# Kernel optimization log

Hardware: AMD Instinct MI355X
Metric: run time of the kernel (lower is better)

## Reference

```python
import jax, jax.numpy as jnp
import numpy as np

N = 1_000_000      # occupied voxels
GRID = 256         # voxel grid extent per axis
K = 27             # 3^3 kernel offsets
CIN, COUT = 2, 16


def _build_nbr_map(coords: np.ndarray) -> np.ndarray:
    """Kernel-offset neighbor map like MinkowskiEngine's kernel map.
    coords: [N,3] unique int voxel coords. Returns [N,K] int32, -1 = no neighbor.
    """
    key = (coords[:, 0] * GRID + coords[:, 1]) * GRID + coords[:, 2]
    order = np.argsort(key)
    skey = key[order]
    offsets = np.array([[dx, dy, dz]
                        for dx in (-1, 0, 1)
                        for dy in (-1, 0, 1)
                        for dz in (-1, 0, 1)], dtype=np.int64)
    nbr = np.full((coords.shape[0], K), -1, dtype=np.int32)
    for k in range(K):
        nc = coords + offsets[k]
        valid = np.all((nc >= 0) & (nc < GRID), axis=1)
        nkey = (nc[:, 0] * GRID + nc[:, 1]) * GRID + nc[:, 2]
        pos = np.clip(np.searchsorted(skey, nkey), 0, coords.shape[0] - 1)
        hit = valid & (skey[pos] == nkey)
        nbr[:, k] = np.where(hit, order[pos].astype(np.int32), -1)
    return nbr


def setup_inputs() -> dict:
    rng = np.random.default_rng(0)
    lin = rng.choice(GRID ** 3, size=N, replace=False)  # unique voxel ids
    coords = np.stack([lin // (GRID * GRID), (lin // GRID) % GRID, lin % GRID],
                      axis=1).astype(np.int64)
    nbr = _build_nbr_map(coords)
    key = jax.random.key(0)
    k1, k2 = jax.random.split(key)
    features = jax.random.normal(k1, (N, CIN), dtype=jnp.float32)
    # MinkowskiConvolution kernel: one [Cin,Cout] matrix per kernel offset, no bias
    kernel = jax.random.normal(k2, (K, CIN, COUT), dtype=jnp.float32) * 0.1
    return {"features": features, "kernel": kernel, "nbr_idx": jnp.asarray(nbr)}


def reference(features, kernel, nbr_idx):
    # gather-GEMM-scatter sparse conv: out[n] = sum_k W_k^T x[nbr(n,k)]
    mask = (nbr_idx >= 0)
    safe = jnp.maximum(nbr_idx, 0)
    gathered = features[safe]                              # [N,K,Cin]
    gathered = gathered * mask[..., None].astype(features.dtype)
    return jnp.einsum('nkc,kcd->nd', gathered, kernel)     # [N,Cout]
```

## Files before the change

kernel.cpp:

```cpp
#include <hip/hip_runtime.h>

#define K_OFF 27
#define CIN   2
#define COUT  16
#define BLK   256
#define WPB   4
#define IPW   (64 * K_OFF)
#define NB    8

typedef __attribute__((address_space(3))) unsigned int lds_u32;
typedef __attribute__((address_space(1))) const unsigned int g_u32;

__global__ __launch_bounds__(256) void pack_feats_kernel(
    const float2* __restrict__ feats2, unsigned* __restrict__ pkf, int n)
{
    const int i = blockIdx.x * 256 + threadIdx.x;
    if (i < n) {
        const float2 f = feats2[i];
        unsigned bx = __float_as_uint(f.x);
        unsigned by = __float_as_uint(f.y);
        bx = (bx + 0x7FFFu + ((bx >> 16) & 1u)) >> 16;
        by = (by + 0x7FFFu + ((by >> 16) & 1u)) >> 16;
        pkf[i] = bx | (by << 16);
    }
}

__global__ __launch_bounds__(BLK, 2) void spconv_kernel(
    const unsigned* __restrict__ pkf,
    const float* __restrict__ w,
    const int*   __restrict__ nbr,
    float*       __restrict__ out,
    int n_pts)
{
    __shared__ int    s_idx[WPB * IPW];
    __shared__ float4 s_w[8 * K_OFF];

    const int t    = threadIdx.x;
    const int lane = t & 63;
    const int wv   = t >> 6;
    const int tile = blockIdx.x * WPB + wv;
    const int p    = tile * 64 + lane;

    if (t < 8 * K_OFF) {
        const int k = t >> 3, q = t & 7;
        s_w[q * K_OFF + k] = reinterpret_cast<const float4*>(w)[t];
    }

    const bool full = ((tile + 1) * 64 <= n_pts);
    if (full) {
        const int* src = nbr + (size_t)tile * IPW;
        int*       dst = s_idx + wv * IPW;
        #pragma unroll
        for (int j = 0; j < 6; ++j) {
            __builtin_amdgcn_global_load_lds(
                (g_u32*)(src + j * 256 + lane * 4),
                (lds_u32*)(dst + j * 256), 16, 0, 0);
        }
        if (lane < 48) {
            __builtin_amdgcn_global_load_lds(
                (g_u32*)(src + 6 * 256 + lane * 4),
                (lds_u32*)(dst + 6 * 256), 16, 0, 0);
        }
    }
    __syncthreads();

    float acc[COUT];
    #pragma unroll
    for (int d = 0; d < COUT; ++d) acc[d] = 0.f;

    const int* rowp = s_idx + wv * IPW + lane * K_OFF;

    unsigned bm = 0;
    if (full) {
        #pragma unroll
        for (int k = 0; k < K_OFF; ++k)
            bm |= (rowp[k] >= 0) ? (1u << k) : 0u;
    }

    int mx = __popc(bm);
    #pragma unroll
    for (int off = 32; off; off >>= 1) mx = max(mx, __shfl_xor(mx, off, 64));

    for (int j0 = 0; j0 < mx; j0 += NB) {
        int   kk[NB]; float fm[NB];
        #pragma unroll
        for (int j = 0; j < NB; ++j) {
            const bool alive = (bm != 0);
            kk[j] = alive ? (int)__builtin_ctz(bm) : 0;
            fm[j] = alive ? 1.0f : 0.0f;
            bm &= bm - 1;
        }
        int idx[NB];
        #pragma unroll
        for (int j = 0; j < NB; ++j) idx[j] = rowp[kk[j]];
        unsigned u[NB];
        #pragma unroll
        for (int j = 0; j < NB; ++j)
            u[j] = pkf[(fm[j] > 0.f && idx[j] > 0) ? idx[j] : 0];
        #pragma unroll
        for (int j = 0; j < NB; ++j) {
            const float fx = __uint_as_float(u[j] << 16) * fm[j];
            const float fy = __uint_as_float(u[j] & 0xFFFF0000u) * fm[j];
            const int k = kk[j];
            #pragma unroll
            for (int q = 0; q < 4; ++q) {
                const float4 wa = s_w[q * K_OFF + k];
                const float4 wb = s_w[(q + 4) * K_OFF + k];
                acc[q*4+0] = fmaf(fy, wb.x, fmaf(fx, wa.x, acc[q*4+0]));
                acc[q*4+1] = fmaf(fy, wb.y, fmaf(fx, wa.y, acc[q*4+1]));
                acc[q*4+2] = fmaf(fy, wb.z, fmaf(fx, wa.z, acc[q*4+2]));
                acc[q*4+3] = fmaf(fy, wb.w, fmaf(fx, wa.w, acc[q*4+3]));
            }
        }
    }

    if (!full) {
        const bool pv = (p < n_pts);
        for (int k = 0; k < K_OFF; ++k) {
            const int idx = pv ? nbr[(size_t)p * K_OFF + k] : -1;
            const float fm2 = (idx >= 0) ? 1.0f : 0.0f;
            const unsigned uu = pkf[idx > 0 ? idx : 0];
            const float fx = __uint_as_float(uu << 16) * fm2;
            const float fy = __uint_as_float(uu & 0xFFFF0000u) * fm2;
            #pragma unroll
            for (int q = 0; q < 4; ++q) {
                const float4 wa = s_w[q * K_OFF + k];
                const float4 wb = s_w[(q + 4) * K_OFF + k];
                acc[q*4+0] = fmaf(fy, wb.x, fmaf(fx, wa.x, acc[q*4+0]));
                acc[q*4+1] = fmaf(fy, wb.y, fmaf(fx, wa.y, acc[q*4+1]));
                acc[q*4+2] = fmaf(fy, wb.z, fmaf(fx, wa.z, acc[q*4+2]));
                acc[q*4+3] = fmaf(fy, wb.w, fmaf(fx, wa.w, acc[q*4+3]));
            }
        }
    }

    if (p < n_pts) {
        float4* o = reinterpret_cast<float4*>(out + (size_t)p * COUT);
        o[0] = make_float4(acc[0],  acc[1],  acc[2],  acc[3]);
        o[1] = make_float4(acc[4],  acc[5],  acc[6],  acc[7]);
        o[2] = make_float4(acc[8],  acc[9],  acc[10], acc[11]);
        o[3] = make_float4(acc[12], acc[13], acc[14], acc[15]);
    }
}

extern "C" void kernel_launch(void* const* d_in, const int* in_sizes, int n_in,
                              void* d_out, int out_size, void* d_ws, size_t ws_size,
                              hipStream_t stream) {
    const float* feats = (const float*)d_in[0];
    const float* w     = (const float*)d_in[1];
    const int*   nbr   = (const int*)d_in[2];
    float*       out   = (float*)d_out;
    unsigned*    pkf   = (unsigned*)d_ws;

    const int n_pts   = in_sizes[0] / CIN;
    const int n_tiles = (n_pts + 63) / 64;
    const int grid    = (n_tiles + WPB - 1) / WPB;

    pack_feats_kernel<<<(n_pts + 255) / 256, 256, 0, stream>>>(
        reinterpret_cast<const float2*>(feats), pkf, n_pts);
    spconv_kernel<<<grid, BLK, 0, stream>>>(pkf, w, nbr, out, n_pts);
}
```

Measured before the change: 53.95 us.

## Pipeline neighbor-map staging and feature gathers in a persistent warp loop

Replaces the one-tile-per-wave kernel with a persistent kernel capped at 512 blocks. Each wave loops over tiles and double-buffers the neighbor-index tile in LDS, issuing async global-to-LDS gathers of the packed features for the next tile while it computes the current one. Partial tiles move to a separate small tail kernel, which adds a launch. The aim is to hide the latency of the index loads and random feature gathers. In exchange it relies on fragile hand-written vmcnt/lgkmcnt waits, uses more LDS per block and may give less occupancy-driven parallelism.

```diff
diff --git a/kernel.cpp b/kernel.cpp
--- a/kernel.cpp
+++ b/kernel.cpp
@@ -25,122 +25,246 @@
     }
 }
 
-__global__ __launch_bounds__(BLK, 2) void spconv_kernel(
+__device__ __forceinline__ void stage_tile(const int* __restrict__ nbr,
+                                           int tile, int* dst, int lane) {
+    const int* src = nbr + (size_t)tile * IPW;
+    #pragma unroll
+    for (int j = 0; j < 6; ++j)
+        __builtin_amdgcn_global_load_lds((g_u32*)(src + j * 256 + lane * 4),
+                                         (lds_u32*)(dst + j * 256), 16, 0, 0);
+    if (lane < 48)
+        __builtin_amdgcn_global_load_lds((g_u32*)(src + 6 * 256 + lane * 4),
+                                         (lds_u32*)(dst + 6 * 256), 16, 0, 0);
+}
+
+#define SCAN_CAP_ISSUE(BUF, GB, KK, IX, NV, MX)                               \
+    {                                                                         \
+        const int* rowp_ = (BUF) + lane * K_OFF;                              \
+        unsigned b_ = 0;                                                      \
+        _Pragma("unroll")                                                     \
+        for (int k2 = 0; k2 < K_OFF; ++k2)                                    \
+            b_ |= (rowp_[k2] >= 0) ? (1u << k2) : 0u;                         \
+        NV = __popc(b_);                                                      \
+        int m_ = NV;                                                          \
+        _Pragma("unroll")                                                     \
+        for (int o_ = 32; o_; o_ >>= 1) m_ = max(m_, __shfl_xor(m_, o_, 64)); \
+        MX = m_;                                                              \
+        _Pragma("unroll")                                                     \
+        for (int j = 0; j < 2 * NB; ++j) {                                    \
+            KK[j] = (b_ != 0) ? (int)__builtin_ctz(b_) : 0;                   \
+            b_ &= b_ - 1;                                                     \
+        }                                                                     \
+        _Pragma("unroll")                                                     \
+        for (int j = 0; j < NB; ++j) {                \
+            const int ii_ = rowp_[KK[NB + j]];                                \
+            IX[j] = (NB + j < NV && ii_ > 0) ? ii_ : 0;                       \
+        }                                                                     \
+        _Pragma("unroll")                                                     \
+        for (int j = 0; j < NB; ++j) {     \
+            const int iv_ = rowp_[KK[j]];                                     \
+            const int sf_ = (j < NV && iv_ > 0) ? iv_ : 0;                    \
+            __builtin_amdgcn_global_load_lds((g_u32*)(pkf + sf_),             \
+                                             (lds_u32*)((GB) + j * 64), 4, 0, 0); \
+        }                                                                     \
+    }
+
+#define FMA_LDS(GB, KK, NV, JOFF)                                             \
+    _Pragma("unroll")                                                         \
+    for (int j = 0; j < NB; ++j) {                                            \
+        const unsigned u_ = (unsigned)(GB)[j * 64 + lane];                    \
+        const float fm_ = ((JOFF) + j < (NV)) ? 1.0f : 0.0f;                  \
+        const float fx = __uint_as_float(u_ << 16) * fm_;                     \
+        const float fy = __uint_as_float(u_ & 0xFFFF0000u) * fm_;             \
+        const int k2 = KK[(JOFF) + j];                                        \
+        _Pragma("unroll")                                                     \
+        for (int q = 0; q < 4; ++q) {                                         \
+            const float4 wa = s_w[q * K_OFF + k2];                            \
+            const float4 wb = s_w[(q + 4) * K_OFF + k2];                      \
+            acc[4*q+0] = fmaf(fy, wb.x, fmaf(fx, wa.x, acc[4*q+0]));          \
+            acc[4*q+1] = fmaf(fy, wb.y, fmaf(fx, wa.y, acc[4*q+1]));          \
+            acc[4*q+2] = fmaf(fy, wb.z, fmaf(fx, wa.z, acc[4*q+2]));          \
+            acc[4*q+3] = fmaf(fy, wb.w, fmaf(fx, wa.w, acc[4*q+3]));          \
+        }                                                                     \
+    }
+
+__global__ __launch_bounds__(BLK, 2) void spconv_pipe_kernel(
     const unsigned* __restrict__ pkf,
-    const float* __restrict__ w,
-    const int*   __restrict__ nbr,
-    float*       __restrict__ out,
-    int n_pts)
+    const float*    __restrict__ w,
+    const int*      __restrict__ nbr,
+    float*          __restrict__ out,
+    int n_tiles)
 {
-    __shared__ int    s_idx[WPB * IPW];
-    __shared__ float4 s_w[8 * K_OFF];
+    __shared__ int    s_idx[WPB * 2 * IPW];
+    __shared__ int    s_g  [WPB * 2 * NB * 64];
+    __shared__ float4 s_w  [8 * K_OFF];
 
     const int t    = threadIdx.x;
     const int lane = t & 63;
     const int wv   = t >> 6;
-    const int tile = blockIdx.x * WPB + wv;
-    const int p    = tile * 64 + lane;
 
     if (t < 8 * K_OFF) {
         const int k = t >> 3, q = t & 7;
         s_w[q * K_OFF + k] = reinterpret_cast<const float4*>(w)[t];
     }
-
-    const bool full = ((tile + 1) * 64 <= n_pts);
-    if (full) {
-        const int* src = nbr + (size_t)tile * IPW;
-        int*       dst = s_idx + wv * IPW;
+    __syncthreads();
+
+    const int wstride = gridDim.x * WPB;
+    int tile = blockIdx.x * WPB + wv;
+    if (tile >= n_tiles) return;
+
+    int* const bufA = s_idx + wv * (2 * IPW);
+    int* const bufB = bufA + IPW;
+    int* const gbA  = s_g + wv * (2 * NB * 64);
+    int* const gbB  = gbA + NB * 64;
+
+    int kk1[2 * NB], ix1[NB], nv1, mx1;
+    int kk2[2 * NB], ix2[NB], nv2, mx2;
+
+    stage_tile(nbr, tile, bufA, lane);
+    asm volatile("s_waitcnt vmcnt(0)" ::: "memory");
+    __builtin_amdgcn_sched_barrier(0);
+    SCAN_CAP_ISSUE(bufA, gbA, kk1, ix1, nv1, mx1)
+    if (tile + wstride < n_tiles) stage_tile(nbr, tile + wstride, bufB, lane);
+
+    int  cur   = 0;
+    bool first = true;
+
+    while (true) {
+        const int  nxt  = tile + wstride;
+        const bool has1 = (nxt < n_tiles);
+        const int  n2   = tile + 2 * wstride;
+        const bool has2 = (n2 < n_tiles);
+
+        int* const bufC = cur ? bufB : bufA;
+        int* const bufN = cur ? bufA : bufB;
+        int* const gbC  = cur ? gbB  : gbA;
+        int* const gbN  = cur ? gbA  : gbB;
+
+        if (first) asm volatile("s_waitcnt vmcnt(0)" ::: "memory");
+        else       asm volatile("s_waitcnt vmcnt(4)" ::: "memory");
+        first = false;
+        __builtin_amdgcn_sched_barrier(0);
+
+        const bool early_stage = has2 && (mx1 <= 2 * NB);
+        if (early_stage) stage_tile(nbr, n2, bufC, lane);
+
+        if (has1) SCAN_CAP_ISSUE(bufN, gbN, kk2, ix2, nv2, mx2)
+
+        float acc[COUT];
         #pragma unroll
-        for (int j = 0; j < 6; ++j) {
-            __builtin_amdgcn_global_load_lds(
-                (g_u32*)(src + j * 256 + lane * 4),
-                (lds_u32*)(dst + j * 256), 16, 0, 0);
+        for (int d = 0; d < COUT; ++d) acc[d] = 0.f;
+
+        FMA_LDS(gbC, kk1, nv1, 0)
+
+        if (mx1 > NB) {
+            asm volatile("s_waitcnt lgkmcnt(0)" ::: "memory");
+            __builtin_amdgcn_sched_barrier(0);
+            #pragma unroll
+            for (int j = 0; j < NB; ++j)
+                __builtin_amdgcn_global_load_lds((g_u32*)(pkf + ix1[j]),
+                                                 (lds_u32*)(gbC + j * 64), 4, 0, 0);
+            asm volatile("s_waitcnt vmcnt(0)" ::: "memory");
+            __builtin_amdgcn_sched_barrier(0);
+            FMA_LDS(gbC, kk1, nv1, NB)
+
+            if (mx1 > 2 * NB) {
+                const int* rowp_ = bufC + lane * K_OFF;
+                unsigned b_ = 0;
+                #pragma unroll
+                for (int k2 = 0; k2 < K_OFF; ++k2)
+                    b_ |= (rowp_[k2] >= 0) ? (1u << k2) : 0u;
+                #pragma unroll
+                for (int j = 0; j < 2 * NB; ++j) b_ &= b_ - 1;
+                int rem = mx1 - 2 * NB;
+                while (rem > 0) {
+                    int kkx[NB]; float fmx[NB];
+                    #pragma unroll
+                    for (int j = 0; j < NB; ++j) {
+                        const bool a_ = (b_ != 0);
+                        kkx[j] = a_ ? (int)__builtin_ctz(b_) : 0;
+                        fmx[j] = a_ ? 1.0f : 0.0f;
+                        b_ &= b_ - 1;
+                    }
+                    asm volatile("s_waitcnt lgkmcnt(0)" ::: "memory");
+                    __builtin_amdgcn_sched_barrier(0);
+                    #pragma unroll
+                    for (int j = 0; j < NB; ++j) {
+                        const int iv_ = rowp_[kkx[j]];
+                        const int sf_ = (fmx[j] > 0.f && iv_ > 0) ? iv_ : 0;
+                        __builtin_amdgcn_global_load_lds((g_u32*)(pkf + sf_),
+                                                         (lds_u32*)(gbC + j * 64), 4, 0, 0);
+                    }
+                    asm volatile("s_waitcnt vmcnt(0)" ::: "memory");
+                    __builtin_amdgcn_sched_barrier(0);
+                    #pragma unroll
+                    for (int j = 0; j < NB; ++j) {
+                        const unsigned u_ = (unsigned)gbC[j * 64 + lane];
+                        const float fx = __uint_as_float(u_ << 16) * fmx[j];
+                        const float fy = __uint_as_float(u_ & 0xFFFF0000u) * fmx[j];
+                        const int k2 = kkx[j];
+                        #pragma unroll
+                        for (int q = 0; q < 4; ++q) {
+                            const float4 wa = s_w[q * K_OFF + k2];
+                            const float4 wb = s_w[(q + 4) * K_OFF + k2];
+                            acc[4*q+0] = fmaf(fy, wb.x, fmaf(fx, wa.x, acc[4*q+0]));
+                            acc[4*q+1] = fmaf(fy, wb.y, fmaf(fx, wa.y, acc[4*q+1]));
+                            acc[4*q+2] = fmaf(fy, wb.z, fmaf(fx, wa.z, acc[4*q+2]));
+                            acc[4*q+3] = fmaf(fy, wb.w, fmaf(fx, wa.w, acc[4*q+3]));
+                        }
+                    }
+                    rem -= NB;
+                }
+                if (has2) stage_tile(nbr, n2, bufC, lane);
+            }
         }
-        if (lane < 48) {
-            __builtin_amdgcn_global_load_lds(
-                (g_u32*)(src + 6 * 256 + lane * 4),
-                (lds_u32*)(dst + 6 * 256), 16, 0, 0);
+
+        {
+            const int p = tile * 64 + lane;
+            float4* o = reinterpret_cast<float4*>(out + (size_t)p * COUT);
+            o[0] = make_float4(acc[0],  acc[1],  acc[2],  acc[3]);
+            o[1] = make_float4(acc[4],  acc[5],  acc[6],  acc[7]);
+            o[2] = make_float4(acc[8],  acc[9],  acc[10], acc[11]);
+            o[3] = make_float4(acc[12], acc[13], acc[14], acc[15]);
         }
-    }
-    __syncthreads();
-
+
+        if (!has1) break;
+
+        #pragma unroll
+        for (int j = 0; j < 2 * NB; ++j) kk1[j] = kk2[j];
+        #pragma unroll
+        for (int j = 0; j < NB; ++j) ix1[j] = ix2[j];
+        nv1 = nv2; mx1 = mx2;
+
+        tile = nxt;
+        cur ^= 1;
+    }
+}
+
+__global__ __launch_bounds__(64) void spconv_tail_kernel(
+    const unsigned* __restrict__ pkf, const float* __restrict__ w,
+    const int* __restrict__ nbr, float* __restrict__ out, int n_pts, int p0)
+{
+    const int p = p0 + threadIdx.x;
+    if (p >= n_pts) return;
     float acc[COUT];
     #pragma unroll
     for (int d = 0; d < COUT; ++d) acc[d] = 0.f;
-
-    const int* rowp = s_idx + wv * IPW + lane * K_OFF;
-
-    unsigned bm = 0;
-    if (full) {
-        #pragma unroll
-        for (int k = 0; k < K_OFF; ++k)
-            bm |= (rowp[k] >= 0) ? (1u << k) : 0u;
-    }
-
-    int mx = __popc(bm);
-    #pragma unroll
-    for (int off = 32; off; off >>= 1) mx = max(mx, __shfl_xor(mx, off, 64));
-
-    for (int j0 = 0; j0 < mx; j0 += NB) {
-        int   kk[NB]; float fm[NB];
-        #pragma unroll
-        for (int j = 0; j < NB; ++j) {
-            const bool alive = (bm != 0);
-            kk[j] = alive ? (int)__builtin_ctz(bm) : 0;
-            fm[j] = alive ? 1.0f : 0.0f;
-            bm &= bm - 1;
+    for (int k = 0; k < K_OFF; ++k) {
+        const int idx = nbr[(size_t)p * K_OFF + k];
+        if (idx >= 0) {
+            const unsigned u = pkf[idx];
+            const float fx = __uint_as_float(u << 16);
+            const float fy = __uint_as_float(u & 0xFFFF0000u);
+            #pragma unroll
+            for (int d = 0; d < COUT; ++d)
+                acc[d] = fmaf(fy, w[k * 32 + 16 + d], fmaf(fx, w[k * 32 + d], acc[d]));
         }
-        int idx[NB];
-        #pragma unroll
-        for (int j = 0; j < NB; ++j) idx[j] = rowp[kk[j]];
-        unsigned u[NB];
-        #pragma unroll
-        for (int j = 0; j < NB; ++j)
-            u[j] = pkf[(fm[j] > 0.f && idx[j] > 0) ? idx[j] : 0];
-        #pragma unroll
-        for (int j = 0; j < NB; ++j) {
-            const float fx = __uint_as_float(u[j] << 16) * fm[j];
-            const float fy = __uint_as_float(u[j] & 0xFFFF0000u) * fm[j];
-            const int k = kk[j];
-            #pragma unroll
-            for (int q = 0; q < 4; ++q) {
-                const float4 wa = s_w[q * K_OFF + k];
-                const float4 wb = s_w[(q + 4) * K_OFF + k];
-                acc[q*4+0] = fmaf(fy, wb.x, fmaf(fx, wa.x, acc[q*4+0]));
-                acc[q*4+1] = fmaf(fy, wb.y, fmaf(fx, wa.y, acc[q*4+1]));
-                acc[q*4+2] = fmaf(fy, wb.z, fmaf(fx, wa.z, acc[q*4+2]));
-                acc[q*4+3] = fmaf(fy, wb.w, fmaf(fx, wa.w, acc[q*4+3]));
-            }
-        }
-    }
-
-    if (!full) {
-        const bool pv = (p < n_pts);
-        for (int k = 0; k < K_OFF; ++k) {
-            const int idx = pv ? nbr[(size_t)p * K_OFF + k] : -1;
-            const float fm2 = (idx >= 0) ? 1.0f : 0.0f;
-            const unsigned uu = pkf[idx > 0 ? idx : 0];
-            const float fx = __uint_as_float(uu << 16) * fm2;
-            const float fy = __uint_as_float(uu & 0xFFFF0000u) * fm2;
-            #pragma unroll
-            for (int q = 0; q < 4; ++q) {
-                const float4 wa = s_w[q * K_OFF + k];
-                const float4 wb = s_w[(q + 4) * K_OFF + k];
-                acc[q*4+0] = fmaf(fy, wb.x, fmaf(fx, wa.x, acc[q*4+0]));
-                acc[q*4+1] = fmaf(fy, wb.y, fmaf(fx, wa.y, acc[q*4+1]));
-                acc[q*4+2] = fmaf(fy, wb.z, fmaf(fx, wa.z, acc[q*4+2]));
-                acc[q*4+3] = fmaf(fy, wb.w, fmaf(fx, wa.w, acc[q*4+3]));
-            }
-        }
-    }
-
-    if (p < n_pts) {
-        float4* o = reinterpret_cast<float4*>(out + (size_t)p * COUT);
-        o[0] = make_float4(acc[0],  acc[1],  acc[2],  acc[3]);
-        o[1] = make_float4(acc[4],  acc[5],  acc[6],  acc[7]);
-        o[2] = make_float4(acc[8],  acc[9],  acc[10], acc[11]);
-        o[3] = make_float4(acc[12], acc[13], acc[14], acc[15]);
-    }
+    }
+    float4* o = reinterpret_cast<float4*>(out + (size_t)p * COUT);
+    o[0] = make_float4(acc[0],  acc[1],  acc[2],  acc[3]);
+    o[1] = make_float4(acc[4],  acc[5],  acc[6],  acc[7]);
+    o[2] = make_float4(acc[8],  acc[9],  acc[10], acc[11]);
+    o[3] = make_float4(acc[12], acc[13], acc[14], acc[15]);
 }
 
 extern "C" void kernel_launch(void* const* d_in, const int* in_sizes, int n_in,
@@ -152,11 +276,18 @@
     float*       out   = (float*)d_out;
     unsigned*    pkf   = (unsigned*)d_ws;
 
-    const int n_pts   = in_sizes[0] / CIN;
-    const int n_tiles = (n_pts + 63) / 64;
-    const int grid    = (n_tiles + WPB - 1) / WPB;
+    const int n_pts  = in_sizes[0] / CIN;
+    const int n_full = n_pts / 64;
+    const int rem    = n_pts % 64;
 
     pack_feats_kernel<<<(n_pts + 255) / 256, 256, 0, stream>>>(
         reinterpret_cast<const float2*>(feats), pkf, n_pts);
-    spconv_kernel<<<grid, BLK, 0, stream>>>(pkf, w, nbr, out, n_pts);
-}
+
+    if (n_full > 0) {
+        int grid = (n_full + WPB - 1) / WPB;
+        if (grid > 512) grid = 512;
+        spconv_pipe_kernel<<<grid, BLK, 0, stream>>>(pkf, w, nbr, out, n_full);
+    }
+    if (rem > 0)
+        spconv_tail_kernel<<<1, 64, 0, stream>>>(pkf, w, nbr, out, n_pts, n_full * 64);
+}
```

Result: slower. 57.11 us (+5.9%).
